# Optimization experiments

Hardware: AMD Instinct MI355X
Metric: run time of the kernel (lower is better)

The kernel has to match this reference:

```python
import jax, jax.numpy as jnp
import numpy as np

PS = 14            # patch size
EMBED = 1024       # vision embed dim
LLM = 2048         # llm embed dim
DS = 2             # downsample factor
B = 8
GRID = 64          # H = W = 64 patches per image
MAX_POS = 4096
ROPE_THETA = 10000.0


def _rope_cache(dim, max_pos, base):
    inv_freq = 1.0 / (base ** (jnp.arange(0, dim, 2, dtype=jnp.float32) / dim))
    t = jnp.arange(max_pos, dtype=jnp.float32)
    freqs = jnp.outer(t, inv_freq)  # [max_pos, dim//2]
    return jnp.cos(freqs), jnp.sin(freqs)


def setup_inputs() -> dict:
    key = jax.random.key(0)
    ks = jax.random.split(key, 5)
    n_total = B * GRID * GRID
    pixel_values = jax.random.normal(ks[0], (n_total, 3, PS, PS), jnp.float32)
    patch_w = jax.random.normal(ks[1], (EMBED, 3, PS, PS), jnp.float32) * (1.0 / np.sqrt(3 * PS * PS))
    patch_b = jax.random.normal(ks[2], (EMBED,), jnp.float32) * 0.02
    dense_w = jax.random.normal(ks[3], (LLM, EMBED, DS, DS), jnp.float32) * (1.0 / np.sqrt(EMBED * DS * DS))
    dense_b = jax.random.normal(ks[4], (LLM,), jnp.float32) * 0.02
    rope_dim = EMBED // 2
    cos_x, sin_x = _rope_cache(rope_dim, MAX_POS, ROPE_THETA)
    cos_y, sin_y = _rope_cache(rope_dim, MAX_POS, ROPE_THETA)
    grid_hw = jnp.full((B, 2), GRID, dtype=jnp.int32)
    return {"pixel_values": pixel_values, "grid_hw": grid_hw,
            "patch_w": patch_w, "patch_b": patch_b,
            "dense_w": dense_w, "dense_b": dense_b,
            "cos_x": cos_x, "sin_x": sin_x, "cos_y": cos_y, "sin_y": sin_y}


def _apply_rotary_1d(x, cos_c, sin_c, pos):
    # x: [N, d], cos_c/sin_c: [max_pos, d//2], pos: [N] int
    c = cos_c[pos]  # gather: [N, d//2]
    s = sin_c[pos]
    x1 = x[:, 0::2]
    x2 = x[:, 1::2]
    o1 = x1 * c - x2 * s
    o2 = x1 * s + x2 * c
    return jnp.stack([o1, o2], axis=-1).reshape(x.shape)  # re-interleave


def _positions(grid_np):
    # grid metadata is static host-side data; build per-patch (x, y) coords
    xs, ys = [], []
    for h, w in grid_np:
        pid = np.arange(h * w)
        xs.append(pid % w)
        ys.append(pid // w)
    return jnp.asarray(np.concatenate(xs)), jnp.asarray(np.concatenate(ys))


def reference(pixel_values, grid_hw, patch_w, patch_b, dense_w, dense_b,
              cos_x, sin_x, cos_y, sin_y):
    grid_np = np.asarray(grid_hw)
    # patchify conv (kernel == stride == patch) is a per-patch linear proj
    pe = jnp.einsum('nchw,echw->ne', pixel_values, patch_w) + patch_b  # [N, E]
    pe = jax.nn.gelu(pe, approximate=False)
    abs_x, abs_y = _positions(grid_np)
    half = EMBED // 2
    p1 = _apply_rotary_1d(pe[:, :half], cos_x, sin_x, abs_x)
    p2 = _apply_rotary_1d(pe[:, half:], cos_y, sin_y, abs_y)
    pe = jnp.concatenate([p1, p2], axis=-1)  # [N, E]
    # per-image downsample conv (kernel == stride == DS): 2x2 block linear
    outs = []
    cur = 0
    for h, w in grid_np:
        x = pe[cur:cur + h * w].reshape(h // DS, DS, w // DS, DS, EMBED)
        o = jnp.einsum('hpwqe,oepq->hwo', x, dense_w) + dense_b
        outs.append(o.reshape(-1, LLM))
        cur += h * w
    return jnp.concatenate(outs, axis=0)
```

## Files before the change

### kernel.cpp

```cpp
#include <hip/hip_runtime.h>
#include <cstdint>


using f16x8 = __attribute__((ext_vector_type(8))) _Float16;
using f16x4 = __attribute__((ext_vector_type(4))) _Float16;
using f32x4 = __attribute__((ext_vector_type(4))) float;

__device__ __forceinline__ void gload_lds16(const void* g, void* l) {
  __builtin_amdgcn_global_load_lds(
      reinterpret_cast<const __attribute__((address_space(1))) unsigned int*>(
          reinterpret_cast<uintptr_t>(g)),
      reinterpret_cast<__attribute__((address_space(3))) unsigned int*>(
          reinterpret_cast<uintptr_t>(l)),
      16, 0, 0);
}

#define BAR   asm volatile("s_barrier" ::: "memory")
#define LGKM0 asm volatile("s_waitcnt lgkmcnt(0)" ::: "memory")
#define VM0   asm volatile("s_waitcnt vmcnt(0)" ::: "memory")

#define KP 640


__global__ void conv_w_kernel(const float* __restrict__ w1,
                              const float* __restrict__ w2,
                              _Float16* __restrict__ h1,
                              _Float16* __restrict__ h2) {
  const int bid = blockIdx.x;
  if (bid < 2560) {
    int i = bid * 256 + threadIdx.x;
    int e = i / KP;
    int k = i - e * KP;
    float v = (k < 588) ? w1[(size_t)e * 588 + k] : 0.0f;
    h1[i] = (_Float16)v;
  } else {
    int j = (bid - 2560) * 256 + threadIdx.x;
    int o = j >> 10;
    int e = j & 1023;
    const float4 v = *(const float4*)(w2 + (size_t)o * 4096 + e * 4);
    h2[(size_t)o * 4096 + e]        = (_Float16)v.x;
    h2[(size_t)o * 4096 + 1024 + e] = (_Float16)v.y;
    h2[(size_t)o * 4096 + 2048 + e] = (_Float16)v.z;
    h2[(size_t)o * 4096 + 3072 + e] = (_Float16)v.w;
  }
}


#define MFMA16(I0, J0, AV, BV)                                                \
  _Pragma("unroll") for (int i_ = 0; i_ < 4; ++i_)                            \
  _Pragma("unroll") for (int j_ = 0; j_ < 2; ++j_)                            \
  _Pragma("unroll") for (int k_ = 0; k_ < 2; ++k_)                            \
      acc[(I0) + i_][(J0) + j_] = __builtin_amdgcn_mfma_f32_16x16x32_f16(     \
          AV[i_][k_], BV[j_][k_], acc[(I0) + i_][(J0) + j_], 0, 0, 0);

#define TILE_BODY(sb)                                                         \
  {                                                                           \
    f16x8 a0[4][2], a1[4][2], vb0[2][2], vb1[2][2];                           \
    _Pragma("unroll") for (int i = 0; i < 4; ++i) {                           \
      a0[i][0] = *(const f16x8*)(lbase + (sb) + aoff + i * 2048 + so0);       \
      a0[i][1] = *(const f16x8*)(lbase + (sb) + aoff + i * 2048 + so1);       \
    }                                                                         \
    _Pragma("unroll") for (int j = 0; j < 2; ++j) {                           \
      vb0[j][0] = *(const f16x8*)(lbase + (sb) + boff + j * 2048 + so0);      \
      vb0[j][1] = *(const f16x8*)(lbase + (sb) + boff + j * 2048 + so1);      \
    }                                                                         \
    MFMA16(0, 0, a0, vb0);                                                    \
    _Pragma("unroll") for (int j = 0; j < 2; ++j) {                           \
      vb1[j][0] = *(const f16x8*)(lbase + (sb) + boff + (2+j) * 2048 + so0);  \
      vb1[j][1] = *(const f16x8*)(lbase + (sb) + boff + (2+j) * 2048 + so1);  \
    }                                                                         \
    MFMA16(0, 2, a0, vb1);                                                    \
    _Pragma("unroll") for (int i = 0; i < 4; ++i) {                           \
      a1[i][0] = *(const f16x8*)(lbase + (sb) + aoff + (4+i) * 2048 + so0);   \
      a1[i][1] = *(const f16x8*)(lbase + (sb) + aoff + (4+i) * 2048 + so1);   \
    }                                                                         \
    MFMA16(4, 2, a1, vb1);                                                    \
    MFMA16(4, 0, a1, vb0);                                                    \
  }


__global__ __launch_bounds__(512, 2) void patch_gemm17(
    const float* __restrict__ pix,
    const _Float16* __restrict__ b1w,
    const float* __restrict__ bias1,
    const float* __restrict__ cosx, const float* __restrict__ sinx,
    const float* __restrict__ cosy, const float* __restrict__ siny,
    _Float16* __restrict__ peM)
{
  __shared__ _Float16 lds[2][256][64];

  const int tid  = threadIdx.x;
  const int lane = tid & 63;
  const int wave = tid >> 6;
  const int wm = wave >> 2, wn = wave & 3;
  const int bm = blockIdx.x, bn = blockIdx.y;
  const int l15 = lane & 15;
  const int g   = lane >> 4;
  const int s7  = l15 & 7;

  const char* lbase = (const char*)lds;
  char*       lw    = (char*)lds;
  const unsigned aoff = (unsigned)(wm * 16384 + l15 * 128);
  const unsigned boff = (unsigned)(32768 + wn * 8192 + l15 * 128);
  const unsigned so0  = (unsigned)(((0 + g) ^ s7) * 16);
  const unsigned so1  = (unsigned)(((4 + g) ^ s7) * 16);

  const int bm256 = bm * 256, bn256 = bn * 256;
  const int srow = wave * 32 + (lane >> 3);
  const int acol = lane & 15;
  const int arw  = wave * 32 + (lane >> 4);

  auto LOADA = [&](int s, float4 (&ar)[8]) {
    const bool full = (s < 9);
#pragma unroll
    for (int u = 0; u < 8; ++u) {
      const int row = arw + u * 4;
      const float* p = pix + (size_t)(bm256 + row) * 588 + s * 64 + acol * 4;
      if (full || acol < 3) ar[u] = *(const float4*)p;
      else ar[u] = make_float4(0.f, 0.f, 0.f, 0.f);
    }
  };
  auto WRITEA = [&](float4 (&ar)[8]) {
    const int c   = acol >> 1;
    const int sub = acol & 1;
#pragma unroll
    for (int u = 0; u < 8; ++u) {
      const int row = arw + u * 4;
      f16x4 v;
      v[0] = (_Float16)ar[u].x; v[1] = (_Float16)ar[u].y;
      v[2] = (_Float16)ar[u].z; v[3] = (_Float16)ar[u].w;
      *(f16x4*)(lw + row * 128 + ((c ^ (row & 7)) * 16 + sub * 8)) = v;
    }
  };
  auto STAGE_B = [&](int s) {
    const int c0 = s * 64;
#pragma unroll
    for (int u = 0; u < 4; ++u) {
      const int row  = srow + u * 8;
      const int gcol = (lane & 7) ^ (row & 7);
      gload_lds16(b1w + (size_t)(bn256 + row) * KP + c0 + gcol * 8,
                  lw + 32768 + (wave * 4 + u) * 1024);
    }
  };

  f32x4 acc[8][4] = {};
  float4 areg[8];

  LOADA(0, areg);
  for (int s = 0; s < 10; ++s) {
    WRITEA(areg);
    STAGE_B(s);
    VM0;
    LGKM0; BAR;
    if (s + 1 < 10) LOADA(s + 1, areg);
    __builtin_amdgcn_s_setprio(1);
    TILE_BODY(0u);
    __builtin_amdgcn_s_setprio(0);
    LGKM0; BAR;
  }

  float* sw = (float*)(lw) + wave * (16 * 65);
  const int md = (lane >> 4) * 4;
  const int rq = lane & 3;
  const int lr = lane >> 2;
#pragma unroll
  for (int p = 0; p < 8; ++p) {
#pragma unroll
    for (int r = 0; r < 4; ++r) {
      const int lrow = md + r;
#pragma unroll
      for (int nf = 0; nf < 4; ++nf)
        sw[lrow * 65 + nf * 16 + l15] = acc[p][nf][r];
    }
    {
      const int m   = bm256 + wm * 128 + p * 16 + lr;
      const int pid = m & 4095;
      const int yy = pid >> 6, xx = pid & 63;
      const int t  = (m >> 12) * 1024 + (yy >> 1) * 32 + (xx >> 1);
      const int pq = (yy & 1) * 2 + (xx & 1);
      const int e0 = bn256 + wn * 64 + rq * 16;
      const int h2 = (e0 >= 512) ? 1 : 0;
      const int idx0 = (h2 ? (e0 - 512) : e0) >> 1;
      const int pos  = h2 ? yy : xx;
      const float* ct = (h2 ? cosy : cosx) + pos * 256 + idx0;
      const float* st = (h2 ? siny : sinx) + pos * 256 + idx0;
      const float4 c0 = *(const float4*)ct, c1 = *(const float4*)(ct + 4);
      const float4 s0 = *(const float4*)st, s1 = *(const float4*)(st + 4);
      const float4 b0 = *(const float4*)(bias1 + e0);
      const float4 b1 = *(const float4*)(bias1 + e0 + 4);
      const float4 b2 = *(const float4*)(bias1 + e0 + 8);
      const float4 b3 = *(const float4*)(bias1 + e0 + 12);
      const float bb[16] = {b0.x,b0.y,b0.z,b0.w, b1.x,b1.y,b1.z,b1.w,
                            b2.x,b2.y,b2.z,b2.w, b3.x,b3.y,b3.z,b3.w};
      float v[16];
#pragma unroll
      for (int j = 0; j < 16; ++j) {
        float x = sw[lr * 65 + rq * 16 + j] + bb[j];
        v[j] = 0.5f * x * (1.0f + erff(x * 0.70710678118654752f));
      }
      const float cc[8] = {c0.x,c0.y,c0.z,c0.w, c1.x,c1.y,c1.z,c1.w};
      const float ss[8] = {s0.x,s0.y,s0.z,s0.w, s1.x,s1.y,s1.z,s1.w};
      _Float16 o[16];
#pragma unroll
      for (int k = 0; k < 8; ++k) {
        o[2*k]   = (_Float16)(v[2*k] * cc[k] - v[2*k+1] * ss[k]);
        o[2*k+1] = (_Float16)(v[2*k] * ss[k] + v[2*k+1] * cc[k]);
      }
      _Float16* dst = peM + (size_t)t * 4096 + pq * 1024 + e0;
      *(f16x8*)dst       = *(const f16x8*)&o[0];
      *(f16x8*)(dst + 8) = *(const f16x8*)&o[8];
    }
  }
}


__global__ __launch_bounds__(512, 2) void dense_gemm9(
    const _Float16* __restrict__ aM,
    const _Float16* __restrict__ bM,
    const float* __restrict__ bias2, float* __restrict__ out)
{
  __shared__ _Float16 lds[2][2][256][64];

  const int tid  = threadIdx.x;
  const int lane = tid & 63;
  const int wave = tid >> 6;
  const int wm = wave >> 2, wn = wave & 3;
  const int bm = blockIdx.x, bn = blockIdx.y;
  const int l15 = lane & 15;
  const int g   = lane >> 4;
  const int s7  = l15 & 7;

  const char* lbase = (const char*)lds;
  char*       lw    = (char*)lds;
  const unsigned aoff = (unsigned)(wm * 16384 + l15 * 128);
  const unsigned boff = (unsigned)(32768 + wn * 8192 + l15 * 128);
  const unsigned so0  = (unsigned)(((0 + g) ^ s7) * 16);
  const unsigned so1  = (unsigned)(((4 + g) ^ s7) * 16);

  const int bm256 = bm * 256, bn256 = bn * 256;
  const int srow = (wave * 4) * 8 + (lane >> 3);

  auto STAGE = [&](int s) {
    char* slot = lw + ((size_t)(s & 1) << 16);
    const int c0 = s * 64;
#pragma unroll
    for (int u = 0; u < 4; ++u) {
      const int row  = srow + u * 8;
      const int gcol = (lane & 7) ^ (row & 7);
      gload_lds16(aM + (size_t)(bm256 + row) * 4096 + c0 + gcol * 8,
                  slot + (wave * 4 + u) * 1024);
      gload_lds16(bM + (size_t)(bn256 + row) * 4096 + c0 + gcol * 8,
                  slot + 32768 + (wave * 4 + u) * 1024);
    }
  };

  f32x4 acc[8][4] = {};

  STAGE(0); VM0; BAR;
#pragma unroll 2
  for (int s = 0; s < 64; ++s) {
    if (s + 1 < 64) STAGE(s + 1);
    const unsigned sb = (unsigned)((s & 1) << 16);
    __builtin_amdgcn_s_setprio(1);
    TILE_BODY(sb);
    __builtin_amdgcn_s_setprio(0);
    LGKM0; VM0; BAR;
  }

  const int md = (lane >> 4) * 4;
  const int r0 = bm256 + wm * 128;
  const int c0 = bn256 + wn * 64;
#pragma unroll
  for (int nf = 0; nf < 4; ++nf) {
    const int o = c0 + nf * 16 + l15;
    const float bs = bias2[o];
#pragma unroll
    for (int mf = 0; mf < 8; ++mf) {
      const int t_ = r0 + mf * 16 + md;
#pragma unroll
      for (int r = 0; r < 4; ++r)
        out[(size_t)(t_ + r) * 2048 + o] = acc[mf][nf][r] + bs;
    }
  }
}


extern "C" void kernel_launch(void* const* d_in, const int* in_sizes, int n_in,
                              void* d_out, int out_size, void* d_ws, size_t ws_size,
                              hipStream_t stream) {
  const float* pix  = (const float*)d_in[0];
  const float* w1   = (const float*)d_in[2];
  const float* b1   = (const float*)d_in[3];
  const float* w2   = (const float*)d_in[4];
  const float* b2   = (const float*)d_in[5];
  const float* cosx = (const float*)d_in[6];
  const float* sinx = (const float*)d_in[7];
  const float* cosy = (const float*)d_in[8];
  const float* siny = (const float*)d_in[9];
  float* out = (float*)d_out;

  _Float16* ws = (_Float16*)d_ws;
  const size_t PE_N  = (size_t)8192 * 4096;
  const size_t B1_N  = (size_t)1024 * KP;
  _Float16* peM  = ws;
  _Float16* b1h  = peM + PE_N;
  _Float16* b2h  = b1h + B1_N;

  conv_w_kernel<<<dim3(2560 + 8192), dim3(256), 0, stream>>>(w1, w2, b1h, b2h);
  patch_gemm17<<<dim3(128, 4), dim3(512), 0, stream>>>(
      pix, b1h, b1, cosx, sinx, cosy, siny, peM);
  dense_gemm9<<<dim3(32, 8), dim3(512), 0, stream>>>(
      peM, b2h, b2, out);
}
```

Before: 251.3 us.

## Stage fp32 pixels directly into LDS via async loads, convert at fragment read

The patch GEMM no longer loads fp32 pixel tiles into registers and converts them to fp16 before writing LDS. Raw fp32 pixel rows now go into LDS through global_load_lds, alongside the weight tile, and are converted to fp16 when the MFMA fragments are read. The K step shrinks from 64 to 32 over 19 iterations, and the weight padding drops from 640 to 608 columns. The aim is to cut register pressure and VALU conversion work in the load path, at the cost of more barrier-synchronised iterations with no double buffering. The last tile's out-of-range pixel reads are clamped to the buffer end.

```diff
diff --git a/kernel.cpp b/kernel.cpp
--- a/kernel.cpp
+++ b/kernel.cpp
@@ -3,7 +3,6 @@
 
 
 using f16x8 = __attribute__((ext_vector_type(8))) _Float16;
-using f16x4 = __attribute__((ext_vector_type(4))) _Float16;
 using f32x4 = __attribute__((ext_vector_type(4))) float;
 
 __device__ __forceinline__ void gload_lds16(const void* g, void* l) {
@@ -19,7 +18,7 @@
 #define LGKM0 asm volatile("s_waitcnt lgkmcnt(0)" ::: "memory")
 #define VM0   asm volatile("s_waitcnt vmcnt(0)" ::: "memory")
 
-#define KP 640
+#define KP1 608
 
 
 __global__ void conv_w_kernel(const float* __restrict__ w1,
@@ -27,14 +26,14 @@
                               _Float16* __restrict__ h1,
                               _Float16* __restrict__ h2) {
   const int bid = blockIdx.x;
-  if (bid < 2560) {
+  if (bid < 2432) {
     int i = bid * 256 + threadIdx.x;
-    int e = i / KP;
-    int k = i - e * KP;
+    int e = i / KP1;
+    int k = i - e * KP1;
     float v = (k < 588) ? w1[(size_t)e * 588 + k] : 0.0f;
     h1[i] = (_Float16)v;
   } else {
-    int j = (bid - 2560) * 256 + threadIdx.x;
+    int j = (bid - 2432) * 256 + threadIdx.x;
     int o = j >> 10;
     int e = j & 1023;
     const float4 v = *(const float4*)(w2 + (size_t)o * 4096 + e * 4);
@@ -79,7 +78,7 @@
   }
 
 
-__global__ __launch_bounds__(512, 2) void patch_gemm17(
+__global__ __launch_bounds__(512, 2) void patch_gemm18(
     const float* __restrict__ pix,
     const _Float16* __restrict__ b1w,
     const float* __restrict__ bias1,
@@ -87,7 +86,7 @@
     const float* __restrict__ cosy, const float* __restrict__ siny,
     _Float16* __restrict__ peM)
 {
-  __shared__ _Float16 lds[2][256][64];
+  __shared__ char lds[49152];
 
   const int tid  = threadIdx.x;
   const int lane = tid & 63;
@@ -98,63 +97,65 @@
   const int g   = lane >> 4;
   const int s7  = l15 & 7;
 
-  const char* lbase = (const char*)lds;
-  char*       lw    = (char*)lds;
-  const unsigned aoff = (unsigned)(wm * 16384 + l15 * 128);
-  const unsigned boff = (unsigned)(32768 + wn * 8192 + l15 * 128);
-  const unsigned so0  = (unsigned)(((0 + g) ^ s7) * 16);
-  const unsigned so1  = (unsigned)(((4 + g) ^ s7) * 16);
+  const char* lbase = lds;
+  char*       lw    = lds;
 
   const int bm256 = bm * 256, bn256 = bn * 256;
-  const int srow = wave * 32 + (lane >> 3);
-  const int acol = lane & 15;
-  const int arw  = wave * 32 + (lane >> 4);
-
-  auto LOADA = [&](int s, float4 (&ar)[8]) {
-    const bool full = (s < 9);
-#pragma unroll
-    for (int u = 0; u < 8; ++u) {
-      const int row = arw + u * 4;
-      const float* p = pix + (size_t)(bm256 + row) * 588 + s * 64 + acol * 4;
-      if (full || acol < 3) ar[u] = *(const float4*)p;
-      else ar[u] = make_float4(0.f, 0.f, 0.f, 0.f);
+  const int arow = wave * 32 + (lane >> 3);
+  const int ac   = lane & 7;
+  const int brow = wave * 32 + (lane >> 2);
+  const int bc   = lane & 3;
+  const size_t PIXB = (size_t)32768 * 588 * 4;
+
+  const unsigned aB   = (unsigned)(wm * 16384 + l15 * 128);
+  const unsigned soA0 = (unsigned)(((2 * g) ^ s7) * 16);
+  const unsigned soA1 = soA0 ^ 16u;
+  const unsigned bB   = (unsigned)(32768 + wn * 4096 + l15 * 64);
+  const unsigned soB  = (unsigned)((g ^ (l15 & 3)) * 16);
+
+  auto STAGE = [&](int s) {
+#pragma unroll
+    for (int u = 0; u < 4; ++u) {
+      const int row  = arow + u * 8;
+      const int gcol = ac ^ (row & 7);
+      size_t ob = (size_t)(bm256 + row) * 2352 + (size_t)s * 128 + gcol * 16;
+      if (ob > PIXB - 16) ob = PIXB - 16;
+      gload_lds16((const char*)pix + ob, lw + (wave * 4 + u) * 1024);
+    }
+#pragma unroll
+    for (int u = 0; u < 2; ++u) {
+      const int row  = brow + u * 16;
+      const int gcol = bc ^ (row & 3);
+      gload_lds16(b1w + (size_t)(bn256 + row) * KP1 + s * 32 + gcol * 8,
+                  lw + 32768 + (wave * 2 + u) * 1024);
     }
   };
-  auto WRITEA = [&](float4 (&ar)[8]) {
-    const int c   = acol >> 1;
-    const int sub = acol & 1;
-#pragma unroll
-    for (int u = 0; u < 8; ++u) {
-      const int row = arw + u * 4;
-      f16x4 v;
-      v[0] = (_Float16)ar[u].x; v[1] = (_Float16)ar[u].y;
-      v[2] = (_Float16)ar[u].z; v[3] = (_Float16)ar[u].w;
-      *(f16x4*)(lw + row * 128 + ((c ^ (row & 7)) * 16 + sub * 8)) = v;
-    }
-  };
-  auto STAGE_B = [&](int s) {
-    const int c0 = s * 64;
-#pragma unroll
-    for (int u = 0; u < 4; ++u) {
-      const int row  = srow + u * 8;
-      const int gcol = (lane & 7) ^ (row & 7);
-      gload_lds16(b1w + (size_t)(bn256 + row) * KP + c0 + gcol * 8,
-                  lw + 32768 + (wave * 4 + u) * 1024);
-    }
-  };
 
   f32x4 acc[8][4] = {};
-  float4 areg[8];
-
-  LOADA(0, areg);
-  for (int s = 0; s < 10; ++s) {
-    WRITEA(areg);
-    STAGE_B(s);
-    VM0;
-    LGKM0; BAR;
-    if (s + 1 < 10) LOADA(s + 1, areg);
+
+  for (int s = 0; s < 19; ++s) {
+    STAGE(s);
+    VM0; BAR;
     __builtin_amdgcn_s_setprio(1);
-    TILE_BODY(0u);
+    f16x8 bf[4];
+#pragma unroll
+    for (int j = 0; j < 4; ++j)
+      bf[j] = *(const f16x8*)(lbase + bB + j * 1024 + soB);
+#pragma unroll
+    for (int i = 0; i < 8; ++i) {
+      const f32x4 lo = *(const f32x4*)(lbase + aB + i * 2048 + soA0);
+      const f32x4 hi = *(const f32x4*)(lbase + aB + i * 2048 + soA1);
+      f16x8 af;
+#pragma unroll
+      for (int q = 0; q < 4; ++q) {
+        af[q]     = (_Float16)lo[q];
+        af[4 + q] = (_Float16)hi[q];
+      }
+#pragma unroll
+      for (int j = 0; j < 4; ++j)
+        acc[i][j] = __builtin_amdgcn_mfma_f32_16x16x32_f16(af, bf[j],
+                                                           acc[i][j], 0, 0, 0);
+    }
     __builtin_amdgcn_s_setprio(0);
     LGKM0; BAR;
   }
@@ -301,13 +302,13 @@
 
   _Float16* ws = (_Float16*)d_ws;
   const size_t PE_N  = (size_t)8192 * 4096;
-  const size_t B1_N  = (size_t)1024 * KP;
+  const size_t B1_N  = (size_t)1024 * KP1;
   _Float16* peM  = ws;
   _Float16* b1h  = peM + PE_N;
   _Float16* b2h  = b1h + B1_N;
 
-  conv_w_kernel<<<dim3(2560 + 8192), dim3(256), 0, stream>>>(w1, w2, b1h, b2h);
-  patch_gemm17<<<dim3(128, 4), dim3(512), 0, stream>>>(
+  conv_w_kernel<<<dim3(2432 + 8192), dim3(256), 0, stream>>>(w1, w2, b1h, b2h);
+  patch_gemm18<<<dim3(128, 4), dim3(512), 0, stream>>>(
       pix, b1h, b1, cosx, sinx, cosy, siny, peM);
   dense_gemm9<<<dim3(32, 8), dim3(512), 0, stream>>>(
       peM, b2h, b2, out);
```

Result: slower. 266.8 us (+6.2%).

## Shrink dense GEMM tile to 128x256 and drop LDS double buffering

Applied to the files above, without the earlier changes.

The dense GEMM tile drops from 256x256 to 128x256 per block, which doubles the grid to 64x8 blocks. The double-buffered LDS prefetch pipeline becomes a single-buffer load-wait-compute loop, so LDS use falls to 48KB. This gives more blocks for occupancy and load balance across CUs, but global-load latency is no longer overlapped with MFMA work, and A/B reuse per block is lower.

```diff
diff --git a/kernel.cpp b/kernel.cpp
--- a/kernel.cpp
+++ b/kernel.cpp
@@ -214,12 +214,12 @@
 }
 
 
-__global__ __launch_bounds__(512, 2) void dense_gemm9(
+__global__ __launch_bounds__(512, 2) void dense_gemm19(
     const _Float16* __restrict__ aM,
     const _Float16* __restrict__ bM,
     const float* __restrict__ bias2, float* __restrict__ out)
 {
-  __shared__ _Float16 lds[2][2][256][64];
+  __shared__ _Float16 lds[3][128][64];
 
   const int tid  = threadIdx.x;
   const int lane = tid & 63;
@@ -232,50 +232,69 @@
 
   const char* lbase = (const char*)lds;
   char*       lw    = (char*)lds;
-  const unsigned aoff = (unsigned)(wm * 16384 + l15 * 128);
-  const unsigned boff = (unsigned)(32768 + wn * 8192 + l15 * 128);
+  const unsigned aoff = (unsigned)(wm * 8192 + l15 * 128);
+  const unsigned boff = (unsigned)(16384 + wn * 8192 + l15 * 128);
   const unsigned so0  = (unsigned)(((0 + g) ^ s7) * 16);
   const unsigned so1  = (unsigned)(((4 + g) ^ s7) * 16);
 
-  const int bm256 = bm * 256, bn256 = bn * 256;
-  const int srow = (wave * 4) * 8 + (lane >> 3);
+  const int bm128 = bm * 128, bn256 = bn * 256;
+  const int sr8 = lane >> 3;
+  const int sc8 = lane & 7;
 
   auto STAGE = [&](int s) {
-    char* slot = lw + ((size_t)(s & 1) << 16);
     const int c0 = s * 64;
 #pragma unroll
+    for (int u = 0; u < 2; ++u) {
+      const int row  = wave * 16 + u * 8 + sr8;
+      const int gcol = sc8 ^ (row & 7);
+      gload_lds16(aM + (size_t)(bm128 + row) * 4096 + c0 + gcol * 8,
+                  lw + (wave * 2 + u) * 1024);
+    }
+#pragma unroll
     for (int u = 0; u < 4; ++u) {
-      const int row  = srow + u * 8;
-      const int gcol = (lane & 7) ^ (row & 7);
-      gload_lds16(aM + (size_t)(bm256 + row) * 4096 + c0 + gcol * 8,
-                  slot + (wave * 4 + u) * 1024);
+      const int row  = wave * 32 + u * 8 + sr8;
+      const int gcol = sc8 ^ (row & 7);
       gload_lds16(bM + (size_t)(bn256 + row) * 4096 + c0 + gcol * 8,
-                  slot + 32768 + (wave * 4 + u) * 1024);
+                  lw + 16384 + (wave * 4 + u) * 1024);
     }
   };
 
-  f32x4 acc[8][4] = {};
-
-  STAGE(0); VM0; BAR;
-#pragma unroll 2
+  f32x4 acc[4][4] = {};
+
   for (int s = 0; s < 64; ++s) {
-    if (s + 1 < 64) STAGE(s + 1);
-    const unsigned sb = (unsigned)((s & 1) << 16);
+    STAGE(s);
+    VM0; BAR;
     __builtin_amdgcn_s_setprio(1);
-    TILE_BODY(sb);
+#pragma unroll
+    for (int ks = 0; ks < 2; ++ks) {
+      const unsigned so = ks ? so1 : so0;
+      f16x8 a[4], b[4];
+#pragma unroll
+      for (int i = 0; i < 4; ++i)
+        a[i] = *(const f16x8*)(lbase + aoff + i * 2048 + so);
+#pragma unroll
+      for (int j = 0; j < 4; ++j)
+        b[j] = *(const f16x8*)(lbase + boff + j * 2048 + so);
+#pragma unroll
+      for (int i = 0; i < 4; ++i)
+#pragma unroll
+        for (int j = 0; j < 4; ++j)
+          acc[i][j] = __builtin_amdgcn_mfma_f32_16x16x32_f16(
+              a[i], b[j], acc[i][j], 0, 0, 0);
+    }
     __builtin_amdgcn_s_setprio(0);
-    LGKM0; VM0; BAR;
+    LGKM0; BAR;
   }
 
   const int md = (lane >> 4) * 4;
-  const int r0 = bm256 + wm * 128;
+  const int r0 = bm128 + wm * 64;
   const int c0 = bn256 + wn * 64;
 #pragma unroll
   for (int nf = 0; nf < 4; ++nf) {
     const int o = c0 + nf * 16 + l15;
     const float bs = bias2[o];
 #pragma unroll
-    for (int mf = 0; mf < 8; ++mf) {
+    for (int mf = 0; mf < 4; ++mf) {
       const int t_ = r0 + mf * 16 + md;
 #pragma unroll
       for (int r = 0; r < 4; ++r)
@@ -309,6 +328,6 @@
   conv_w_kernel<<<dim3(2560 + 8192), dim3(256), 0, stream>>>(w1, w2, b1h, b2h);
   patch_gemm17<<<dim3(128, 4), dim3(512), 0, stream>>>(
       pix, b1h, b1, cosx, sinx, cosy, siny, peM);
-  dense_gemm9<<<dim3(32, 8), dim3(512), 0, stream>>>(
+  dense_gemm19<<<dim3(64, 8), dim3(512), 0, stream>>>(
       peM, b2h, b2, out);
 }
```

Result: slower. 264.2 us (+5.1%).
